# Kernel tuning notes

Measured on AMD Instinct MI355X. Metric: run time of the kernel, lower is better.

Reference implementation:

```python
import jax, jax.numpy as jnp
import numpy as np

B, C, H, W = 1, 512, 64, 64
HEADS, DH = 8, 64
DI = HEADS * DH          # 512 = heads * dim_head
SW = 8                   # sliding window size
CB = 16                  # compress block size
SB = 2                   # selection block size
NSEL = 2                 # num selected blocks
N = H * W                # 4096 tokens
NCB = N // CB            # 256 compress blocks
NFB = N // SB            # 2048 fine (selection) blocks
NEG = jnp.finfo(jnp.float32).min


def setup_inputs() -> dict:
    key = jax.random.key(0)
    ks = jax.random.split(key, 24)
    rn = lambda k, shape, s=0.03: jax.random.normal(k, shape, jnp.float32) * s
    return dict(
        x=jax.random.normal(ks[0], (B, C, H, W), jnp.float32),
        w_in=rn(ks[1], (C, C)), b_in=jnp.zeros((C,), jnp.float32),
        g_norm=jnp.ones((C,), jnp.float32),
        wq=rn(ks[2], (DI, C)), wk=rn(ks[3], (DI, C)), wv=rn(ks[4], (DI, C)),
        k_pos=rn(ks[5], (HEADS, CB, DH), 0.02), v_pos=rn(ks[6], (HEADS, CB, DH), 0.02),
        mem_k=rn(ks[7], (HEADS, 1, DH), 0.02), mem_v=rn(ks[8], (HEADS, 1, DH), 0.02),
        kc_w1=rn(ks[9], (CB * DH, CB * DH)), kc_b1=jnp.zeros((CB * DH,), jnp.float32),
        kc_w2=rn(ks[10], (DH, CB * DH)), kc_b2=jnp.zeros((DH,), jnp.float32),
        vc_w1=rn(ks[11], (CB * DH, CB * DH)), vc_b1=jnp.zeros((CB * DH,), jnp.float32),
        vc_w2=rn(ks[12], (DH, CB * DH)), vc_b2=jnp.zeros((DH,), jnp.float32),
        w_strat=rn(ks[13], (3 * HEADS, C)), b_strat=jnp.zeros((3 * HEADS,), jnp.float32),
        w_comb=rn(ks[14], (C, DI)),
        w_out=rn(ks[15], (C, C)), b_out=jnp.zeros((C,), jnp.float32),
    )


def _rope(x):
    # rotary-embedding-torch default: theta=10000, interleaved pairs
    d = x.shape[-1]
    inv = 1.0 / (10000.0 ** (jnp.arange(0, d, 2, dtype=jnp.float32) / d))
    ang = jnp.arange(x.shape[-2], dtype=jnp.float32)[:, None] * inv  # (n, d/2)
    cos = jnp.repeat(jnp.cos(ang), 2, axis=-1)
    sin = jnp.repeat(jnp.sin(ang), 2, axis=-1)
    xp = x.reshape(x.shape[:-1] + (d // 2, 2))
    xr = jnp.stack((-xp[..., 1], xp[..., 0]), axis=-1).reshape(x.shape)
    return x * cos + xr * sin


def reference(x, w_in, b_in, g_norm, wq, wk, wv, k_pos, v_pos, mem_k, mem_v,
              kc_w1, kc_b1, kc_w2, kc_b2, vc_w1, vc_b1, vc_w2, vc_b2,
              w_strat, b_strat, w_comb, w_out, b_out):
    scale = DH ** -0.5
    # proj_in (1x1 conv) then flatten to sequence (b, n, c); residual uses this
    xs = jnp.einsum('bchw,oc->bohw', x, w_in) + b_in[None, :, None, None]
    seq = xs.reshape(B, C, N).transpose(0, 2, 1)
    # RMSNorm
    h = seq * jax.lax.rsqrt(jnp.mean(seq * seq, -1, keepdims=True) + 1e-6) * g_norm
    # qkv -> (b, heads, n, d)
    q = (h @ wq.T).reshape(B, N, HEADS, DH).transpose(0, 2, 1, 3)
    k = (h @ wk.T).reshape(B, N, HEADS, DH).transpose(0, 2, 1, 3)
    v = (h @ wv.T).reshape(B, N, HEADS, DH).transpose(0, 2, 1, 3)

    # ---- 1. compressed attention (block compression MLP + mem kv) ----
    kin = (k + jnp.tile(k_pos, (1, NCB, 1))[None]).reshape(B, HEADS, NCB, CB * DH)
    vin = (v + jnp.tile(v_pos, (1, NCB, 1))[None]).reshape(B, HEADS, NCB, CB * DH)
    ck = jax.nn.relu(kin @ kc_w1.T + kc_b1) @ kc_w2.T + kc_b2   # (b,h,NCB,d)
    cv = jax.nn.relu(vin @ vc_w1.T + vc_b1) @ vc_w2.T + vc_b2
    ck = jnp.concatenate([jnp.broadcast_to(mem_k[None], (B, HEADS, 1, DH)), ck], axis=2)
    cv = jnp.concatenate([jnp.broadcast_to(mem_v[None], (B, HEADS, 1, DH)), cv], axis=2)
    ck_seq = jnp.concatenate([jnp.array([-1]), (jnp.arange(NCB) + 1) * CB - 1])
    cmask = ck_seq[None, :] < jnp.arange(N)[:, None]             # (N, NCB+1), True=attend
    csim = jnp.einsum('bhid,bhjd->bhij', q, ck) * scale
    csim = jnp.where(cmask[None, None], csim, NEG)
    compressed_out = jnp.einsum('bhij,bhjd->bhid', jax.nn.softmax(csim, axis=-1), cv)

    # rotary positions for fine + sliding branches
    rq, rk = _rope(q), _rope(k)

    # ---- 2. fine selection attention ----
    # importance at fine-block granularity; since SB divides CB, each fine block
    # maps to exactly one compress block (equivalent to repeat->mask->mean in torch)
    imp = csim[..., 1:]                                          # drop mem kv logits
    fb_of = jnp.arange(NFB) // (CB // SB)
    imp_fine = imp[..., fb_of]                                   # (b,h,N,NFB)
    blk_causal = jnp.arange(NFB)[None, :] < (jnp.arange(N) // SB)[:, None]
    imp_fine = jnp.where(blk_causal[None, None], imp_fine, -jnp.inf)
    logits = jnp.concatenate([jnp.full((B, HEADS, N, 1), -1e3, jnp.float32), imp_fine], axis=-1)
    probs = jax.nn.softmax(logits, axis=-1)[..., 1:]             # (b,h,N,NFB)
    sel_val, sel_idx = jax.lax.top_k(probs, NSEL)                # (b,h,N,NSEL)
    diag_idx = jnp.broadcast_to((jnp.arange(N) // SB)[None, None, :, None], (B, HEADS, N, 1))
    sel_idx = jnp.concatenate([sel_idx, diag_idx], axis=-1)      # append own (diagonal) block
    fmask_sel = jnp.repeat((sel_val > 1e-10)[..., None], SB, axis=-1)   # (b,h,N,NSEL,SB)
    diag_mask = jnp.arange(SB)[None, :] <= (jnp.arange(N) % SB)[:, None]  # within-block causal
    diag_mask = jnp.broadcast_to(diag_mask[None, None, :, None, :], (B, HEADS, N, 1, SB))
    fmask = jnp.concatenate([fmask_sel, diag_mask], axis=-2).reshape(B, HEADS, N, (NSEL + 1) * SB)
    fk_blk = rk.reshape(B, HEADS, NFB, SB, DH)
    fv_blk = v.reshape(B, HEADS, NFB, SB, DH)
    idx = sel_idx.reshape(B, HEADS, N * (NSEL + 1))[..., None, None]
    fk = jnp.take_along_axis(fk_blk, idx, axis=2).reshape(B, HEADS, N, (NSEL + 1) * SB, DH)
    fv = jnp.take_along_axis(fv_blk, idx, axis=2).reshape(B, HEADS, N, (NSEL + 1) * SB, DH)
    fsim = jnp.einsum('bhid,bhijd->bhij', rq, fk) * scale
    fsim = jnp.where(fmask, fsim, NEG)
    fine_out = jnp.einsum('bhij,bhijd->bhid', jax.nn.softmax(fsim, axis=-1), fv)

    # ---- 3. sliding window attention (causal, exact window: 0 <= i-j <= SW) ----
    kp = jnp.pad(rk, ((0, 0), (0, 0), (SW, 0), (0, 0)))
    vp = jnp.pad(v, ((0, 0), (0, 0), (SW, 0), (0, 0)))
    widx = jnp.arange(N)[:, None] + jnp.arange(SW + 1)[None, :]  # indices into padded seq
    kw = kp[:, :, widx]                                          # (b,h,N,SW+1,d)
    vw = vp[:, :, widx]
    wvalid = (jnp.arange(N)[:, None] - SW + jnp.arange(SW + 1)[None, :]) >= 0
    ssim = jnp.einsum('bhid,bhijd->bhij', rq, kw) * scale
    ssim = jnp.where(wvalid[None, None], ssim, NEG)
    slide_out = jnp.einsum('bhij,bhijd->bhid', jax.nn.softmax(ssim, axis=-1), vw)

    # ---- combine the three strategies with learned sigmoid gates ----
    gates = jax.nn.sigmoid(h @ w_strat.T + b_strat).reshape(B, N, HEADS, 3).transpose(0, 2, 1, 3)
    out = gates[..., 0:1] * compressed_out + gates[..., 1:2] * fine_out + gates[..., 2:3] * slide_out
    out = out.transpose(0, 2, 1, 3).reshape(B, N, DI) @ w_comb.T  # merge heads + combine
    out2d = out.transpose(0, 2, 1).reshape(B, C, H, W)
    return jnp.einsum('bchw,oc->bohw', out2d, w_out) + b_out[None, :, None, None] + xs
```

## Files before the change

kernel.cpp:

```cpp
#include <hip/hip_runtime.h>
#include <hip/hip_bf16.h>
#include <math.h>

typedef __attribute__((ext_vector_type(8))) short s8v;
typedef __attribute__((ext_vector_type(8))) _Float16 h8v;
typedef __attribute__((ext_vector_type(4))) float f4v;
typedef __hip_bfloat16 bf16;

#define NEGF (-3.40282346638528859812e+38f)
#define QSMEM 20480
#define BSMEM 20480

enum { EPI_F32 = 0, EPI_BIAS, EPI_BRELU_BF16, EPI_BF16, EPI_FINAL };

__device__ __forceinline__ float wred_sum(float v) {
#pragma unroll
  for (int m = 1; m < 64; m <<= 1) v += __shfl_xor(v, m, 64);
  return v;
}

template <int EPI>
__device__ __forceinline__ void bgemm_body(char* smem, int bx, int by, int bz,
    const bf16* __restrict__ A, const bf16* __restrict__ B, void* __restrict__ C,
    int K, int ldC, long sA, long sB, long sC,
    const float* __restrict__ bias, const void* __restrict__ aux) {
  short (*Ahs)[2560] = (short(*)[2560])smem;
  short (*Bhs)[2560] = (short(*)[2560])(smem + 2 * 2560 * 2);
  const short* ah = (const short*)A + (long)bz * sA;
  const short* bh = (const short*)B + (long)bz * sB;
  int tid = threadIdx.x;
  int wv_ = tid >> 6, lane = tid & 63;
  int lrow = tid >> 2, lcol = (tid & 3) << 3;
  int lidx = lrow * 40 + lcol;
  long abase = (long)(bx * 64 + lrow) * K + lcol;
  long bbase = (long)(by * 64 + lrow) * K + lcol;
  int frow = lane & 15, fk = (lane >> 4) << 3;
  int aoff = (wv_ * 16 + frow) * 40 + fk;
  f4v acc[4] = {};
  {
    s8v avh = *(const s8v*)&ah[abase];
    s8v bvh = *(const s8v*)&bh[bbase];
    *(s8v*)&Ahs[0][lidx] = avh;
    *(s8v*)&Bhs[0][lidx] = bvh;
  }
  __syncthreads();
  int nit = K >> 5, buf = 0;
  s8v rAa, rAb, rBa, rBb;
  if (nit > 1) {
    rAa = *(const s8v*)&ah[abase + 32];
    rAb = *(const s8v*)&bh[bbase + 32];
  }
#define B_DSMFMA                                                       \
  {                                                                    \
    s8v afh = *(const s8v*)&Ahs[buf][aoff];                            \
    _Pragma("unroll") for (int nt = 0; nt < 4; nt++) {                 \
      s8v bfh = *(const s8v*)&Bhs[buf][(nt * 16 + frow) * 40 + fk];    \
      acc[nt] = __builtin_amdgcn_mfma_f32_16x16x32_bf16(afh, bfh, acc[nt], 0, 0, 0); \
    }                                                                  \
  }
  for (int it = 0; it < nit; it += 2) {
    if (it + 2 < nit) {
      long ko = (long)(it + 2) << 5;
      rBa = *(const s8v*)&ah[abase + ko];
      rBb = *(const s8v*)&bh[bbase + ko];
    }
    B_DSMFMA
    if (it + 1 < nit) {
      *(s8v*)&Ahs[buf ^ 1][lidx] = rAa;
      *(s8v*)&Bhs[buf ^ 1][lidx] = rAb;
      __syncthreads();
      buf ^= 1;
      if (it + 3 < nit) {
        long ko = (long)(it + 3) << 5;
        rAa = *(const s8v*)&ah[abase + ko];
        rAb = *(const s8v*)&bh[bbase + ko];
      }
      B_DSMFMA
      if (it + 2 < nit) {
        *(s8v*)&Ahs[buf ^ 1][lidx] = rBa;
        *(s8v*)&Bhs[buf ^ 1][lidx] = rBb;
        __syncthreads();
        buf ^= 1;
      }
    }
  }
#undef B_DSMFMA
  int rb = bx * 64 + wv_ * 16 + ((lane >> 4) << 2);
#pragma unroll
  for (int nt = 0; nt < 4; nt++) {
    int gn = by * 64 + nt * 16 + (lane & 15);
#pragma unroll
    for (int rg = 0; rg < 4; rg++) {
      int gm = rb + rg;
      float v = acc[nt][rg];
      long ci = (long)bz * sC + (long)gm * ldC + gn;
      if (EPI == EPI_F32) ((float*)C)[ci] = v;
      else if (EPI == EPI_BIAS) ((float*)C)[ci] = v + bias[gn];
      else if (EPI == EPI_BRELU_BF16) ((bf16*)C)[ci] = __float2bfloat16(fmaxf(v + bias[gn], 0.f));
      else if (EPI == EPI_BF16) ((bf16*)C)[ci] = __float2bfloat16(v);
      else if (EPI == EPI_FINAL)
        ((float*)C)[ci] = v + bias[gm] + ((const float*)aux)[(long)gn * 512 + gm];
    }
  }
}


#define HX_DECL                                                     \
  short* L = (short*)smem;                                          \
  const int MS = 64 * 40;                                           \
  int tid = threadIdx.x;                                            \
  int wv = tid >> 6, lane = tid & 63;                               \
  int lrow = tid >> 2, lcol = (tid & 3) << 3;                       \
  int frow = lane & 15, fk = (lane >> 4) << 3;                      \
  int aoff = (wv * 16 + frow) * 40 + fk;                            \
  int soff = lrow * 40 + lcol;                                      \
  f4v acc0[4] = {}, accx[4] = {}, acc2[4] = {};

#define HX_STAGE0                                                   \
  {                                                                 \
    *(h8v*)&L[0 * MS + soff] = *(const h8v*)&Ah[abase];             \
    *(h8v*)&L[1 * MS + soff] = *(const h8v*)&Al[abase];             \
    *(h8v*)&L[2 * MS + soff] = *(const h8v*)&Bh[bbase];             \
    *(h8v*)&L[3 * MS + soff] = *(const h8v*)&Bl[bbase];             \
  }                                                                 \
  __syncthreads();

#define HX_DSMFMA                                                   \
  {                                                                 \
    h8v ah = *(const h8v*)&L[aoff];                                 \
    h8v al = *(const h8v*)&L[MS + aoff];                            \
    _Pragma("unroll") for (int nt = 0; nt < 4; nt++) {              \
      int bo = 2 * MS + (nt * 16 + frow) * 40 + fk;                 \
      h8v bh = *(const h8v*)&L[bo];                                 \
      h8v bl = *(const h8v*)&L[bo + MS];                            \
      acc0[nt] = __builtin_amdgcn_mfma_f32_16x16x32_f16(ah, bh, acc0[nt], 0, 0, 0); \
      accx[nt] = __builtin_amdgcn_mfma_f32_16x16x32_f16(ah, bl, accx[nt], 0, 0, 0); \
      accx[nt] = __builtin_amdgcn_mfma_f32_16x16x32_f16(al, bh, accx[nt], 0, 0, 0); \
      acc2[nt] = __builtin_amdgcn_mfma_f32_16x16x32_f16(al, bl, acc2[nt], 0, 0, 0); \
    }                                                               \
  }

#define HX_LOOP(NIT)                                                \
  h8v rAa, rAb, rAc, rAd, rBa, rBb, rBc, rBd;                       \
  if ((NIT) > 1) {                                                  \
    rAa = *(const h8v*)&Ah[abase + 32];                             \
    rAb = *(const h8v*)&Al[abase + 32];                             \
    rAc = *(const h8v*)&Bh[bbase + 32];                             \
    rAd = *(const h8v*)&Bl[bbase + 32];                             \
  }                                                                 \
  for (int it = 0; it < (NIT); it += 2) {                           \
    if (it + 2 < (NIT)) {                                           \
      long ko = (long)(it + 2) << 5;                                \
      rBa = *(const h8v*)&Ah[abase + ko];                           \
      rBb = *(const h8v*)&Al[abase + ko];                           \
      rBc = *(const h8v*)&Bh[bbase + ko];                           \
      rBd = *(const h8v*)&Bl[bbase + ko];                           \
    }                                                               \
    HX_DSMFMA                                                       \
    if (it + 1 < (NIT)) {                                           \
      __syncthreads();                                              \
      *(h8v*)&L[soff] = rAa;                                        \
      *(h8v*)&L[MS + soff] = rAb;                                   \
      *(h8v*)&L[2 * MS + soff] = rAc;                               \
      *(h8v*)&L[3 * MS + soff] = rAd;                               \
      __syncthreads();                                              \
      if (it + 3 < (NIT)) {                                         \
        long ko = (long)(it + 3) << 5;                              \
        rAa = *(const h8v*)&Ah[abase + ko];                         \
        rAb = *(const h8v*)&Al[abase + ko];                         \
        rAc = *(const h8v*)&Bh[bbase + ko];                         \
        rAd = *(const h8v*)&Bl[bbase + ko];                         \
      }                                                             \
      HX_DSMFMA                                                     \
      if (it + 2 < (NIT)) {                                         \
        __syncthreads();                                            \
        *(h8v*)&L[soff] = rBa;                                      \
        *(h8v*)&L[MS + soff] = rBb;                                 \
        *(h8v*)&L[2 * MS + soff] = rBc;                             \
        *(h8v*)&L[3 * MS + soff] = rBd;                             \
        __syncthreads();                                            \
      }                                                             \
    }                                                               \
  }

#define HX_COMBINE(nt, rg) \
  (acc0[nt][rg] + (accx[nt][rg] + acc2[nt][rg] * (1.f / 4096.f)) * (1.f / 4096.f))

__device__ __forceinline__ void qk_f16_body(char* smem, int bx, int by,
    const _Float16* __restrict__ Ah, const _Float16* __restrict__ Al,
    const _Float16* __restrict__ Bh, const _Float16* __restrict__ Bl,
    _Float16* __restrict__ qhh, _Float16* __restrict__ qhl,
    _Float16* __restrict__ kinh, _Float16* __restrict__ kinl,
    float* __restrict__ rq, float* __restrict__ rk, const float* __restrict__ kpos,
    const float2* __restrict__ ropet) {
  HX_DECL
  long abase = (long)(bx * 64 + lrow) * 512 + lcol;
  long bbase = (long)(by * 64 + lrow) * 512 + lcol;
  HX_STAGE0
  HX_LOOP(16)
  bool isq = by < 8;
  int h = by & 7;
  int rb = wv * 16 + ((lane >> 4) << 2);
#pragma unroll
  for (int nt = 0; nt < 4; nt++) {
    int dloc = nt * 16 + frow;
    int d2 = dloc >> 1;
#pragma unroll
    for (int rg = 0; rg < 4; rg++) {
      int n = bx * 64 + rb + rg;
      float vf = HX_COMBINE(nt, rg);
      float2 cs = ropet[(long)n * 32 + d2];
      float sv = cs.x, cv = cs.y;
      float vp = __shfl_xor(vf, 1, 64);
      float rr = (dloc & 1) ? (vf * cv + vp * sv) : (vf * cv - vp * sv);
      long oi = ((long)h * 4096 + n) * 64 + dloc;
      if (isq) {
        _Float16 hi = (_Float16)vf;
        qhh[oi] = hi;
        qhl[oi] = (_Float16)((vf - (float)hi) * 4096.f);
        rq[oi] = rr;
      } else {
        rk[oi] = rr;
        float kv = vf + kpos[(h * 16 + (n & 15)) * 64 + dloc];
        _Float16 khi = (_Float16)kv;
        long ki = (((long)h * 256 + (n >> 4)) * 16 + (n & 15)) * 64 + dloc;
        kinh[ki] = khi;
        kinl[ki] = (_Float16)((kv - (float)khi) * 4096.f);
      }
    }
  }
}

__device__ __forceinline__ void hx_conv_body(char* smem, int bx, int by,
    const _Float16* __restrict__ Ah, const _Float16* __restrict__ Al,
    const _Float16* __restrict__ Bh, const _Float16* __restrict__ Bl,
    float* __restrict__ C, const float* __restrict__ bias) {
  HX_DECL
  long abase = (long)(bx * 64 + lrow) * 512 + lcol;
  long bbase = (long)(by * 64 + lrow) * 512 + lcol;
  HX_STAGE0
  HX_LOOP(16)
  int rb = bx * 64 + wv * 16 + ((lane >> 4) << 2);
#pragma unroll
  for (int nt = 0; nt < 4; nt++) {
    int gn = by * 64 + nt * 16 + frow;
#pragma unroll
    for (int rg = 0; rg < 4; rg++) {
      int gm = rb + rg;
      C[(long)gm * 512 + gn] = HX_COMBINE(nt, rg) + bias[gn];
    }
  }
}

__device__ __forceinline__ void hx_mlp1_body(char* smem, int bx, int by,
    const _Float16* __restrict__ Ah, const _Float16* __restrict__ Al,
    const _Float16* __restrict__ Bh, const _Float16* __restrict__ Bl,
    _Float16* __restrict__ Ch, _Float16* __restrict__ Cl, const float* __restrict__ bias) {
  HX_DECL
  long abase = (long)(bx * 64 + lrow) * 1024 + lcol;
  long bbase = (long)(by * 64 + lrow) * 1024 + lcol;
  HX_STAGE0
  HX_LOOP(32)
  int rb = bx * 64 + wv * 16 + ((lane >> 4) << 2);
#pragma unroll
  for (int nt = 0; nt < 4; nt++) {
    int gn = by * 64 + nt * 16 + frow;
#pragma unroll
    for (int rg = 0; rg < 4; rg++) {
      int gm = rb + rg;
      float v = fmaxf(HX_COMBINE(nt, rg) + bias[gn], 0.f);
      _Float16 hi = (_Float16)v;
      long ci = (long)gm * 1024 + gn;
      Ch[ci] = hi;
      Cl[ci] = (_Float16)((v - (float)hi) * 4096.f);
    }
  }
}

__device__ __forceinline__ void hx_ksplit_body(char* smem, int bx, int by,
    const _Float16* __restrict__ Ah, const _Float16* __restrict__ Al,
    const _Float16* __restrict__ Bh, const _Float16* __restrict__ Bl,
    float* __restrict__ P) {
  HX_DECL
  long kbeg = (long)by << 7;
  long abase = (long)(bx * 64 + lrow) * 1024 + kbeg + lcol;
  long bbase = (long)lrow * 1024 + kbeg + lcol;
  HX_STAGE0
  HX_LOOP(4)
  float* p = P + (long)by * 131072;
  int rb = bx * 64 + wv * 16 + ((lane >> 4) << 2);
#pragma unroll
  for (int nt = 0; nt < 4; nt++) {
    int gn = nt * 16 + frow;
#pragma unroll
    for (int rg = 0; rg < 4; rg++) {
      int gm = rb + rg;
      p[(long)gm * 64 + gn] = HX_COMBINE(nt, rg);
    }
  }
}

__device__ __forceinline__ void hx_csim_body(char* smem, int bx, int by, int bz,
    const _Float16* __restrict__ Ah, const _Float16* __restrict__ Al,
    const _Float16* __restrict__ Bh, const _Float16* __restrict__ Bl,
    float* __restrict__ C) {
  HX_DECL
  long abase = ((long)bz * 4096 + bx * 64 + lrow) * 64 + lcol;
  long bbase = ((long)bz * 320 + by * 64 + lrow) * 64 + lcol;
  HX_STAGE0
  HX_LOOP(2)
  int rb = bx * 64 + wv * 16 + ((lane >> 4) << 2);
#pragma unroll
  for (int nt = 0; nt < 4; nt++) {
    int gn = by * 64 + nt * 16 + frow;
#pragma unroll
    for (int rg = 0; rg < 4; rg++) {
      int gm = rb + rg;
      C[((long)bz * 4096 + gm) * 320 + gn] = HX_COMBINE(nt, rg) * 0.125f;
    }
  }
}

__device__ __forceinline__ void prep_elem(long i,
    const float* __restrict__ wq, const float* __restrict__ wk, const float* __restrict__ wv,
    const float* __restrict__ wst, const float* __restrict__ bst,
    const float* __restrict__ kc_w1, const float* __restrict__ kc_w2,
    const float* __restrict__ vc_w1, const float* __restrict__ vc_w2, const float* __restrict__ w_comb,
    const float* __restrict__ w_out, _Float16* __restrict__ wqkh, _Float16* __restrict__ wqkl,
    bf16* __restrict__ wvs, float* __restrict__ bias2,
    _Float16* __restrict__ kw1h, _Float16* __restrict__ kw1l,
    _Float16* __restrict__ kw2h, _Float16* __restrict__ kw2l, bf16* __restrict__ vw1b,
    bf16* __restrict__ vw2b, bf16* __restrict__ wcombb, bf16* __restrict__ woutb) {
  if (i < 524288) {
    int r = (int)(i >> 9), c = (int)(i & 511);
    float w = (r < 512) ? wq[i] : wk[(r - 512) * 512 + c];
    _Float16 hi = (_Float16)w;
    wqkh[i] = hi;
    wqkl[i] = (_Float16)((w - (float)hi) * 4096.f);
    return;
  }
  i -= 524288;
  if (i < 294912) {
    int r = (int)(i >> 9), c = (int)(i & 511);
    float v = 0.f;
    if (r < 512) v = wv[i];
    else if (r < 536) v = wst[(r - 512) * 512 + c];
    wvs[i] = __float2bfloat16(v);
    if (i < 576) bias2[i] = (i >= 512 && i < 536) ? bst[i - 512] : 0.f;
    return;
  }
  i -= 294912;
  if (i < 1048576) {
    float w = kc_w1[i];
    _Float16 hi = (_Float16)w;
    kw1h[i] = hi;
    kw1l[i] = (_Float16)((w - (float)hi) * 4096.f);
    return;
  }
  i -= 1048576;
  if (i < 65536) {
    float w = kc_w2[i];
    _Float16 hi = (_Float16)w;
    kw2h[i] = hi;
    kw2l[i] = (_Float16)((w - (float)hi) * 4096.f);
    return;
  }
  i -= 65536;
  if (i < 1048576) { vw1b[i] = __float2bfloat16(vc_w1[i]); return; }
  i -= 1048576;
  if (i < 65536) { vw2b[i] = __float2bfloat16(vc_w2[i]); return; }
  i -= 65536;
  if (i < 262144) { wcombb[i] = __float2bfloat16(w_comb[i]); return; }
  i -= 262144;
  if (i < 262144) woutb[i] = __float2bfloat16(w_out[i]);
}
#define PREP_TOTAL 3571712l

template <int EPI>
__global__ __launch_bounds__(256) void gemm_bt(
    const bf16* __restrict__ A, const bf16* __restrict__ B, void* __restrict__ C,
    int K, int ldC, long sA, long sB, long sC,
    const float* __restrict__ bias, const void* __restrict__ aux) {
  __shared__ char smem[BSMEM];
  bgemm_body<EPI>(smem, blockIdx.x, blockIdx.y, blockIdx.z, A, B, C, K, ldC, sA, sB, sC, bias, aux);
}

__global__ __launch_bounds__(256) void k_conv_prep(
    const _Float16* __restrict__ xth, const _Float16* __restrict__ xtl,
    const _Float16* __restrict__ winh, const _Float16* __restrict__ winl,
    float* __restrict__ xsf, const float* __restrict__ b_in,
    const float* __restrict__ wq, const float* __restrict__ wk, const float* __restrict__ wv,
    const float* __restrict__ wst, const float* __restrict__ bst,
    const float* __restrict__ kc_w1, const float* __restrict__ kc_w2,
    const float* __restrict__ vc_w1, const float* __restrict__ vc_w2, const float* __restrict__ w_comb,
    const float* __restrict__ w_out, _Float16* __restrict__ wqkh, _Float16* __restrict__ wqkl,
    bf16* __restrict__ wvs, float* __restrict__ bias2,
    _Float16* __restrict__ kw1h, _Float16* __restrict__ kw1l,
    _Float16* __restrict__ kw2h, _Float16* __restrict__ kw2l, bf16* __restrict__ vw1b,
    bf16* __restrict__ vw2b, bf16* __restrict__ wcombb, bf16* __restrict__ woutb) {
  __shared__ char smem[QSMEM];
  if (blockIdx.y < 8) {
    hx_conv_body(smem, blockIdx.x, blockIdx.y, xth, xtl, winh, winl, xsf, b_in);
  } else {
    long base = (((long)(blockIdx.y - 8) * 64 + blockIdx.x) * 256) + threadIdx.x;
    for (long i = base; i < PREP_TOTAL; i += 16l * 64 * 256)
      prep_elem(i, wq, wk, wv, wst, bst, kc_w1, kc_w2, vc_w1, vc_w2, w_comb, w_out,
                wqkh, wqkl, wvs, bias2, kw1h, kw1l, kw2h, kw2l, vw1b, vw2b, wcombb, woutb);
  }
}

__global__ __launch_bounds__(256) void k_fused_qk_t2(
    const _Float16* __restrict__ hhi, const _Float16* __restrict__ hlo,
    const _Float16* __restrict__ wqkh, const _Float16* __restrict__ wqkl,
    _Float16* __restrict__ qhh, _Float16* __restrict__ qhl,
    _Float16* __restrict__ kinh, _Float16* __restrict__ kinl,
    float* __restrict__ rq, float* __restrict__ rk, const float* __restrict__ kpos,
    const float2* __restrict__ ropet,
    const bf16* __restrict__ hbf, const bf16* __restrict__ wvs, float* __restrict__ T2,
    const float* __restrict__ bias2) {
  __shared__ char smem[QSMEM];
  if (blockIdx.y >= 16) {
    bgemm_body<EPI_BIAS>(smem, blockIdx.x, blockIdx.y - 16, 0, hbf, wvs, T2, 512, 576, 0, 0, 0, bias2,
                         nullptr);
    return;
  }
  qk_f16_body(smem, blockIdx.x, blockIdx.y, hhi, hlo, wqkh, wqkl, qhh, qhl, kinh, kinl, rq, rk, kpos,
              ropet);
}

__global__ void k_repackV(const float* __restrict__ T2, const float* __restrict__ vpos,
                          float* __restrict__ vvv, bf16* __restrict__ vin) {
  int e = blockIdx.x * 256 + threadIdx.x;
  int d = e & 63, n = (e >> 6) & 4095, h = e >> 18;
  float v0 = T2[(long)n * 576 + h * 64 + d];
  vvv[((long)h * 4096 + n) * 64 + d] = v0;
  vin[(((long)h * 256 + (n >> 4)) * 16 + (n & 15)) * 64 + d] =
      __float2bfloat16(v0 + vpos[(h * 16 + (n & 15)) * 64 + d]);
}

__global__ __launch_bounds__(256) void k_fused_mlp1(
    const _Float16* __restrict__ kinh, const _Float16* __restrict__ kinl,
    const _Float16* __restrict__ kw1h, const _Float16* __restrict__ kw1l,
    _Float16* __restrict__ hidh, _Float16* __restrict__ hidl, const float* __restrict__ kb1,
    const bf16* __restrict__ vin, const bf16* __restrict__ vw1,
    bf16* __restrict__ hidv, const float* __restrict__ vb1) {
  __shared__ char smem[QSMEM];
  if (blockIdx.y < 16)
    hx_mlp1_body(smem, blockIdx.x, blockIdx.y, kinh, kinl, kw1h, kw1l, hidh, hidl, kb1);
  else
    bgemm_body<EPI_BRELU_BF16>(smem, blockIdx.x, blockIdx.y - 16, 0, vin, vw1, hidv, 1024, 1024, 0, 0, 0,
                               vb1, nullptr);
}

__global__ __launch_bounds__(256) void k_fused_mlp2(
    const _Float16* __restrict__ hidh, const _Float16* __restrict__ hidl,
    const _Float16* __restrict__ kw2h, const _Float16* __restrict__ kw2l, float* __restrict__ kpart,
    const bf16* __restrict__ hidv, const bf16* __restrict__ vw2, float* __restrict__ cvc,
    const float* __restrict__ vb2) {
  __shared__ char smem[QSMEM];
  if (blockIdx.y < 8)
    hx_ksplit_body(smem, blockIdx.x, blockIdx.y, hidh, hidl, kw2h, kw2l, kpart);
  else
    bgemm_body<EPI_BIAS>(smem, blockIdx.x, 0, 0, hidv, vw2, cvc, 1024, 64, 0, 0, 0, vb2, nullptr);
}

__global__ __launch_bounds__(256) void k_csim(
    const _Float16* __restrict__ qhh, const _Float16* __restrict__ qhl,
    const _Float16* __restrict__ ckbh, const _Float16* __restrict__ ckbl, float* __restrict__ csim) {
  if (blockIdx.y * 64 > blockIdx.x * 4 + 3) return;
  __shared__ char smem[QSMEM];
  hx_csim_body(smem, blockIdx.x, blockIdx.y, blockIdx.z, qhh, qhl, ckbh, ckbl, csim);
}

__global__ void k_transpose16(const float* __restrict__ x, _Float16* __restrict__ xth,
                              _Float16* __restrict__ xtl,
                              const float* __restrict__ w_in, _Float16* __restrict__ winh,
                              _Float16* __restrict__ winl, float2* __restrict__ ropet) {
  if (blockIdx.y == 16) {
    int tid = threadIdx.y * 32 + threadIdx.x;
    long base = (long)blockIdx.x * 256 + tid;
    for (long i = base; i < 393216; i += 128l * 256) {
      if (i < 262144) {
        float w = w_in[i];
        _Float16 hi = (_Float16)w;
        winh[i] = hi;
        winl[i] = (_Float16)((w - (float)hi) * 4096.f);
      } else {
        int idx = (int)(i - 262144);
        int d2 = idx & 31, n = idx >> 5;
        float inv = exp2f((float)d2 * -0.4152410118609203f);
        float sv, cv;
        sincosf((float)n * inv, &sv, &cv);
        ropet[idx] = make_float2(sv, cv);
      }
    }
    return;
  }
  __shared__ float t[32][33];
  int n0 = blockIdx.x * 32, c0 = blockIdx.y * 32;
  int tx = threadIdx.x, ty = threadIdx.y;
#pragma unroll
  for (int r = ty; r < 32; r += 8) t[r][tx] = x[(long)(c0 + r) * 4096 + n0 + tx];
  __syncthreads();
#pragma unroll
  for (int r = ty; r < 32; r += 8) {
    float v = t[tx][r];
    _Float16 hi = (_Float16)v;
    long o = (long)(n0 + r) * 512 + c0 + tx;
    xth[o] = hi;
    xtl[o] = (_Float16)((v - (float)hi) * 4096.f);
  }
}

__global__ __launch_bounds__(256) void k_rmsnorm(const float* __restrict__ xs, const float* __restrict__ g,
                                                 _Float16* __restrict__ hhi, _Float16* __restrict__ hlo,
                                                 bf16* __restrict__ hbf) {
  int n = blockIdx.x, t = threadIdx.x;
  const float* row = xs + (long)n * 512;
  double a = (double)row[t], b = (double)row[t + 256];
  double ss = a * a + b * b;
#pragma unroll
  for (int m = 1; m < 64; m <<= 1) ss += __shfl_xor(ss, m, 64);
  __shared__ double red[4];
  if ((t & 63) == 0) red[t >> 6] = ss;
  __syncthreads();
  double tot = red[0] + red[1] + red[2] + red[3];
  double r = 1.0 / sqrt(tot / 512.0 + 1e-6);
  double h0 = a * r * (double)g[t], h1 = b * r * (double)g[t + 256];
  long o = (long)n * 512 + t;
  float f0 = (float)h0, f1 = (float)h1;
  _Float16 a0 = (_Float16)f0, a1 = (_Float16)f1;
  hhi[o] = a0;
  hhi[o + 256] = a1;
  hlo[o] = (_Float16)((f0 - (float)a0) * 4096.f);
  hlo[o + 256] = (_Float16)((f1 - (float)a1) * 4096.f);
  hbf[o] = __float2bfloat16(f0);
  hbf[o + 256] = __float2bfloat16(f1);
}

__global__ void k_repackB(const float* __restrict__ kpart, const float* __restrict__ cvc,
                          const float* __restrict__ mem_k, const float* __restrict__ mem_v,
                          const float* __restrict__ kb2, _Float16* __restrict__ ckbh,
                          _Float16* __restrict__ ckbl, bf16* __restrict__ cvtb) {
  int g = blockIdx.x * 256 + threadIdx.x;
  if (g < 8 * 320 * 64) {
    int d = g & 63, j = (g >> 6) % 320, h = g / (320 * 64);
    float vf = 0.f;
    if (j == 0) vf = mem_k[h * 64 + d];
    else if (j < 257) {
      long ri = ((long)h * 256 + (j - 1)) * 64 + d;
      double s = 0.0;
#pragma unroll
      for (int p = 0; p < 8; p++) s += (double)kpart[(long)p * 131072 + ri];
      vf = (float)(s + (double)kb2[d]);
    }
    _Float16 hi = (_Float16)vf;
    ckbh[g] = hi;
    ckbl[g] = (_Float16)((vf - (float)hi) * 4096.f);
  }
  if (g < 8 * 64 * 288) {
    int j = g % 288, d = (g / 288) & 63, h = g / (288 * 64);
    float v = 0.f;
    if (j == 0) v = mem_v[h * 64 + d];
    else if (j < 257) v = cvc[((long)h * 256 + (j - 1)) * 64 + d];
    cvtb[g] = __float2bfloat16(v);
  }
}

__global__ __launch_bounds__(256) void k_selsm(const float* __restrict__ csim, bf16* __restrict__ pb,
                                               int4* __restrict__ selb) {
  int r = blockIdx.x * 4 + (threadIdx.x >> 6);
  int lane = threadIdx.x & 63;
  int i = r & 4095;
  const float* row = csim + (long)r * 320;
  int nv = i / 16 + 1;
  float s[5], e[5];
  float mx = -INFINITY;
#pragma unroll
  for (int t = 0; t < 5; t++) {
    int j = lane + 64 * t;
    float v = (j < nv) ? row[j] : -INFINITY;
    s[t] = v;
    mx = fmaxf(mx, v);
  }
#pragma unroll
  for (int m = 1; m < 64; m <<= 1) mx = fmaxf(mx, __shfl_xor(mx, m, 64));
  float sum = 0.f;
#pragma unroll
  for (int t = 0; t < 5; t++) {
    int j = lane + 64 * t;
    e[t] = (j < nv) ? __expf(s[t] - mx) : 0.f;
    sum += e[t];
  }
  sum = wred_sum(sum);
  float rinv = 1.f / sum;
  bf16* prow = pb + (long)r * 288;
#pragma unroll
  for (int t = 0; t < 5; t++) {
    int j = lane + 64 * t;
    if (j < 288) prow[j] = __float2bfloat16((j < nv) ? e[t] * rinv : 0.f);
  }
  int nvb = i >> 1;
  int nmv = (nvb + 7) >> 3;
  float vm[4];
  float bestv = -INFINITY;
  int bestm = 0x7fffffff;
#pragma unroll
  for (int t = 0; t < 4; t++) {
    int m = lane + 64 * t;
    float v = -INFINITY;
    if (m < nmv) v = (m + 1 < nv) ? row[m + 1] : NEGF;
    vm[t] = v;
    if (v > bestv) { bestv = v; bestm = m; }
  }
#pragma unroll
  for (int mk = 1; mk < 64; mk <<= 1) {
    float ov = __shfl_xor(bestv, mk, 64);
    int om = __shfl_xor(bestm, mk, 64);
    if (ov > bestv || (ov == bestv && om < bestm)) { bestv = ov; bestm = om; }
  }
  int m0 = bestm;
  int cnt0 = min(8, nvb - 8 * m0);
  float rv = -INFINITY;
  int rm = 0x7fffffff;
#pragma unroll
  for (int t = 0; t < 4; t++) {
    int m = lane + 64 * t;
    if (m != m0 && vm[t] > rv) { rv = vm[t]; rm = m; }
  }
#pragma unroll
  for (int mk = 1; mk < 64; mk <<= 1) {
    float ov = __shfl_xor(rv, mk, 64);
    int om = __shfl_xor(rm, mk, 64);
    if (ov > rv || (ov == rv && om < rm)) { rv = ov; rm = om; }
  }
  float Ml = fmaxf(-1000.f, bestv);
  float z = 0.f;
#pragma unroll
  for (int t = 0; t < 4; t++) {
    int m = lane + 64 * t;
    if (m < nmv) z += (float)min(8, nvb - 8 * m) * expf(vm[t] - Ml);
  }
  z = wred_sum(z) + expf(-1000.f - Ml);
  int fb0 = 0, fb1 = 0, mk0 = 0, mk1 = 0;
  if (nmv > 0) {
    float sv0 = expf(bestv - Ml) / z;
    fb0 = 8 * m0;
    mk0 = sv0 > 1e-10f;
    if (cnt0 >= 2) { fb1 = fb0 + 1; mk1 = mk0; }
    else if (nmv > 1) {
      float sv1 = expf(rv - Ml) / z;
      fb1 = 8 * rm;
      mk1 = sv1 > 1e-10f;
    }
  }
  if (lane == 0) selb[r] = make_int4(fb0, fb1, mk0, mk1);
}

__global__ __launch_bounds__(256) void k_fineslide(const float* __restrict__ rq, const float* __restrict__ rk,
                                                   const float* __restrict__ vv, const float* __restrict__ co,
                                                   const int4* __restrict__ selb, const float* __restrict__ T2,
                                                   bf16* __restrict__ comb) {
  int r = blockIdx.x * 4 + (threadIdx.x >> 6);
  int d = threadIdx.x & 63;
  int h = r >> 12, i = r & 4095;
  long hb = (long)h * 4096 * 64;
  float qd = rq[hb + (long)i * 64 + d];
  int4 s4 = selb[r];
  int dg = i >> 1;
  int tok[6] = {2 * s4.x, 2 * s4.x + 1, 2 * s4.y, 2 * s4.y + 1, 2 * dg, 2 * dg + 1};
  int ok6[6] = {s4.z, s4.z, s4.w, s4.w, 1, (i & 1)};
  float sim[6], val[6];
#pragma unroll
  for (int j = 0; j < 6; j++) {
    float kd = rk[hb + (long)tok[j] * 64 + d];
    val[j] = vv[hb + (long)tok[j] * 64 + d];
    float p = wred_sum(qd * kd);
    sim[j] = ok6[j] ? p * 0.125f : NEGF;
  }
  float mx = sim[0];
#pragma unroll
  for (int j = 1; j < 6; j++) mx = fmaxf(mx, sim[j]);
  float den = 0.f, fo = 0.f;
#pragma unroll
  for (int j = 0; j < 6; j++) {
    float e_ = __expf(sim[j] - mx);
    den += e_;
    fo += e_ * val[j];
  }
  fo /= den;
  float ssim[9], sval[9];
#pragma unroll
  for (int t = 0; t < 9; t++) {
    int tk = i - 8 + t;
    int okt = tk >= 0;
    int tc = okt ? tk : 0;
    float kd = rk[hb + (long)tc * 64 + d];
    sval[t] = okt ? vv[hb + (long)tc * 64 + d] : 0.f;
    float p = wred_sum(qd * kd);
    ssim[t] = okt ? p * 0.125f : NEGF;
  }
  float mx2 = ssim[8];
#pragma unroll
  for (int t = 0; t < 8; t++) mx2 = fmaxf(mx2, ssim[t]);
  float den2 = 0.f, so = 0.f;
#pragma unroll
  for (int t = 0; t < 9; t++) {
    float e_ = __expf(ssim[t] - mx2);
    den2 += e_;
    so += e_ * sval[t];
  }
  so /= den2;
  const float* gb = T2 + (long)i * 576 + 512 + h * 3;
  float g0 = 1.f / (1.f + __expf(-gb[0]));
  float g1 = 1.f / (1.f + __expf(-gb[1]));
  float g2 = 1.f / (1.f + __expf(-gb[2]));
  float cd = co[hb + (long)i * 64 + d];
  comb[(long)i * 512 + h * 64 + d] = __float2bfloat16(g0 * cd + g1 * fo + g2 * so);
}

extern "C" void kernel_launch(void* const* d_in, const int* in_sizes, int n_in, void* d_out, int out_size,
                              void* d_ws, size_t ws_size, hipStream_t stream) {
  (void)in_sizes; (void)n_in; (void)out_size; (void)ws_size;
  const float* x = (const float*)d_in[0];
  const float* w_in = (const float*)d_in[1];
  const float* b_in = (const float*)d_in[2];
  const float* g_norm = (const float*)d_in[3];
  const float* wq = (const float*)d_in[4];
  const float* wk = (const float*)d_in[5];
  const float* wv = (const float*)d_in[6];
  const float* k_pos = (const float*)d_in[7];
  const float* v_pos = (const float*)d_in[8];
  const float* mem_k = (const float*)d_in[9];
  const float* mem_v = (const float*)d_in[10];
  const float* kc_w1 = (const float*)d_in[11];
  const float* kc_b1 = (const float*)d_in[12];
  const float* kc_w2 = (const float*)d_in[13];
  const float* kc_b2 = (const float*)d_in[14];
  const float* vc_w1 = (const float*)d_in[15];
  const float* vc_b1 = (const float*)d_in[16];
  const float* vc_w2 = (const float*)d_in[17];
  const float* vc_b2 = (const float*)d_in[18];
  const float* w_strat = (const float*)d_in[19];
  const float* b_strat = (const float*)d_in[20];
  const float* w_comb = (const float*)d_in[21];
  const float* w_out = (const float*)d_in[22];
  const float* b_out = (const float*)d_in[23];

  char* wsp = (char*)d_ws;
  size_t off = 0;
  auto alloc = [&](size_t b) -> void* {
    void* p = wsp + off;
    off += (b + 255) & ~(size_t)255;
    return p;
  };
  float* xsf = (float*)alloc(4096l * 512 * 4);
  _Float16* hhi = (_Float16*)alloc(4096l * 512 * 2);
  _Float16* hlo = (_Float16*)alloc(4096l * 512 * 2);
  bf16* hbf = (bf16*)alloc(4096l * 512 * 2);
  _Float16* winh = (_Float16*)alloc(512l * 512 * 2);
  _Float16* winl = (_Float16*)alloc(512l * 512 * 2);
  _Float16* wqkh = (_Float16*)alloc(1024l * 512 * 2);
  _Float16* wqkl = (_Float16*)alloc(1024l * 512 * 2);
  bf16* wvs = (bf16*)alloc(576l * 512 * 2);
  float* bias2 = (float*)alloc(576 * 4);
  float2* ropet = (float2*)alloc(4096l * 32 * 8);
  float* T2 = (float*)alloc(4096l * 576 * 4);
  float* csim = (float*)alloc(8l * 4096 * 320 * 4);
  _Float16* qhh = (_Float16*)alloc(8l * 4096 * 64 * 2);
  _Float16* qhl = (_Float16*)alloc(8l * 4096 * 64 * 2);
  float* rq = (float*)alloc(8l * 4096 * 64 * 4);
  float* rk = (float*)alloc(8l * 4096 * 64 * 4);
  float* vvb = (float*)alloc(8l * 4096 * 64 * 4);
  char* xthl = (char*)alloc(2l * 4096 * 512 * 2);
  _Float16* xth = (_Float16*)xthl;
  _Float16* xtl = xth + 4096l * 512;
  _Float16* hidh = xth;
  _Float16* hidl = xtl;
  char* kinpb = (char*)alloc(2048l * 1024 * 8 + 2048l * 1024 * 2);
  _Float16* kinh = (_Float16*)kinpb;
  _Float16* kinl = kinh + 2048l * 1024;
  bf16* vinb = (bf16*)(kinpb + 2l * 2048 * 1024 * 2);
  bf16* pb = (bf16*)kinpb;
  _Float16* kw1h = (_Float16*)alloc(1024l * 1024 * 2);
  _Float16* kw1l = (_Float16*)alloc(1024l * 1024 * 2);
  _Float16* kw2h = (_Float16*)alloc(64l * 1024 * 2);
  _Float16* kw2l = (_Float16*)alloc(64l * 1024 * 2);
  bf16* vw1b = (bf16*)alloc(1024l * 1024 * 2);
  bf16* vw2b = (bf16*)alloc(64l * 1024 * 2);
  bf16* hidv = (bf16*)alloc(2048l * 1024 * 2);
  float* cvc = (float*)alloc(2048l * 64 * 4);
  _Float16* ckbh = (_Float16*)alloc(8l * 320 * 64 * 2);
  _Float16* ckbl = (_Float16*)alloc(8l * 320 * 64 * 2);
  bf16* cvtb = (bf16*)alloc(8l * 64 * 288 * 2);
  int4* selb = (int4*)alloc(32768l * 16);
  float* co = (float*)alloc(8l * 4096 * 64 * 4);
  bf16* comb = (bf16*)alloc(4096l * 512 * 2);
  bf16* zb = (bf16*)alloc(4096l * 512 * 2);
  bf16* wcombb = (bf16*)alloc(512l * 512 * 2);
  bf16* woutb = (bf16*)alloc(512l * 512 * 2);
  float* kpart = (float*)alloc(8l * 2048 * 64 * 4);

  k_transpose16<<<dim3(128, 17), dim3(32, 8), 0, stream>>>(x, xth, xtl, w_in, winh, winl, ropet);
  k_conv_prep<<<dim3(64, 24), 256, 0, stream>>>(xth, xtl, winh, winl, xsf, b_in, wq, wk, wv, w_strat,
                                                b_strat, kc_w1, kc_w2, vc_w1, vc_w2, w_comb, w_out,
                                                wqkh, wqkl, wvs, bias2, kw1h, kw1l, kw2h, kw2l,
                                                vw1b, vw2b, wcombb, woutb);
  k_rmsnorm<<<4096, 256, 0, stream>>>(xsf, g_norm, hhi, hlo, hbf);
  k_fused_qk_t2<<<dim3(64, 25, 1), 256, 0, stream>>>(hhi, hlo, wqkh, wqkl, qhh, qhl, kinh, kinl, rq, rk,
                                                     k_pos, ropet, hbf, wvs, T2, bias2);
  k_repackV<<<8192, 256, 0, stream>>>(T2, v_pos, vvb, vinb);
  k_fused_mlp1<<<dim3(32, 32, 1), 256, 0, stream>>>(kinh, kinl, kw1h, kw1l, hidh, hidl, kc_b1, vinb, vw1b,
                                                    hidv, vc_b1);
  k_fused_mlp2<<<dim3(32, 9, 1), 256, 0, stream>>>(hidh, hidl, kw2h, kw2l, kpart, hidv, vw2b, cvc, vc_b2);
  k_repackB<<<640, 256, 0, stream>>>(kpart, cvc, mem_k, mem_v, kc_b2, ckbh, ckbl, cvtb);
  k_csim<<<dim3(64, 5, 8), 256, 0, stream>>>(qhh, qhl, ckbh, ckbl, csim);
  k_selsm<<<8192, 256, 0, stream>>>(csim, pb, selb);
  gemm_bt<EPI_F32><<<dim3(64, 1, 8), 256, 0, stream>>>(pb, cvtb, co, 288, 64, 4096l * 288, 64l * 288,
                                                       4096l * 64, nullptr, nullptr);
  k_fineslide<<<8192, 256, 0, stream>>>(rq, rk, vvb, co, selb, T2, comb);
  gemm_bt<EPI_BF16><<<dim3(64, 8, 1), 256, 0, stream>>>(comb, wcombb, zb, 512, 512, 0, 0, 0, nullptr, nullptr);
  gemm_bt<EPI_FINAL><<<dim3(8, 64, 1), 256, 0, stream>>>(woutb, zb, d_out, 512, 4096, 0, 0, 0, b_out, xsf);
}
```

Baseline: 325.6 us.

## Fuse compressed-similarity GEMM into selection softmax kernel and deepen MLP2 k-split

Removes the separate csim GEMM kernel and its large fp32 csim buffer. The selection/softmax kernel now computes each 16-row query tile's similarities directly with split-f16 MFMAs into shared memory, then runs the softmax and top-block selection from LDS. This avoids writing and re-reading a roughly 42 MB intermediate, at the cost of fewer MFMA tiles per wave and per-row serial work inside each block. Separately, the k-split for the second key-compression MLP is doubled from 8 to 16 partitions for more parallelism, which means more partial sums for repackB to reduce.

```diff
diff --git a/kernel.cpp b/kernel.cpp
--- a/kernel.cpp
+++ b/kernel.cpp
@@ -178,7 +178,7 @@
         *(h8v*)&L[MS + soff] = rBb;                                 \
         *(h8v*)&L[2 * MS + soff] = rBc;                             \
         *(h8v*)&L[3 * MS + soff] = rBd;                             \
-        __syncthreads();                                            \
+      __syncthreads();                                              \
       }                                                             \
     }                                                               \
   }
@@ -282,11 +282,11 @@
     const _Float16* __restrict__ Bh, const _Float16* __restrict__ Bl,
     float* __restrict__ P) {
   HX_DECL
-  long kbeg = (long)by << 7;
+  long kbeg = (long)by << 6;
   long abase = (long)(bx * 64 + lrow) * 1024 + kbeg + lcol;
   long bbase = (long)lrow * 1024 + kbeg + lcol;
   HX_STAGE0
-  HX_LOOP(4)
+  HX_LOOP(2)
   float* p = P + (long)by * 131072;
   int rb = bx * 64 + wv * 16 + ((lane >> 4) << 2);
 #pragma unroll
@@ -296,27 +296,6 @@
     for (int rg = 0; rg < 4; rg++) {
       int gm = rb + rg;
       p[(long)gm * 64 + gn] = HX_COMBINE(nt, rg);
-    }
-  }
-}
-
-__device__ __forceinline__ void hx_csim_body(char* smem, int bx, int by, int bz,
-    const _Float16* __restrict__ Ah, const _Float16* __restrict__ Al,
-    const _Float16* __restrict__ Bh, const _Float16* __restrict__ Bl,
-    float* __restrict__ C) {
-  HX_DECL
-  long abase = ((long)bz * 4096 + bx * 64 + lrow) * 64 + lcol;
-  long bbase = ((long)bz * 320 + by * 64 + lrow) * 64 + lcol;
-  HX_STAGE0
-  HX_LOOP(2)
-  int rb = bx * 64 + wv * 16 + ((lane >> 4) << 2);
-#pragma unroll
-  for (int nt = 0; nt < 4; nt++) {
-    int gn = by * 64 + nt * 16 + frow;
-#pragma unroll
-    for (int rg = 0; rg < 4; rg++) {
-      int gm = rb + rg;
-      C[((long)bz * 4096 + gm) * 320 + gn] = HX_COMBINE(nt, rg) * 0.125f;
     }
   }
 }
@@ -458,18 +437,10 @@
     const bf16* __restrict__ hidv, const bf16* __restrict__ vw2, float* __restrict__ cvc,
     const float* __restrict__ vb2) {
   __shared__ char smem[QSMEM];
-  if (blockIdx.y < 8)
+  if (blockIdx.y < 16)
     hx_ksplit_body(smem, blockIdx.x, blockIdx.y, hidh, hidl, kw2h, kw2l, kpart);
   else
     bgemm_body<EPI_BIAS>(smem, blockIdx.x, 0, 0, hidv, vw2, cvc, 1024, 64, 0, 0, 0, vb2, nullptr);
-}
-
-__global__ __launch_bounds__(256) void k_csim(
-    const _Float16* __restrict__ qhh, const _Float16* __restrict__ qhl,
-    const _Float16* __restrict__ ckbh, const _Float16* __restrict__ ckbl, float* __restrict__ csim) {
-  if (blockIdx.y * 64 > blockIdx.x * 4 + 3) return;
-  __shared__ char smem[QSMEM];
-  hx_csim_body(smem, blockIdx.x, blockIdx.y, blockIdx.z, qhh, qhl, ckbh, ckbl, csim);
 }
 
 __global__ void k_transpose16(const float* __restrict__ x, _Float16* __restrict__ xth,
@@ -551,7 +522,7 @@
       long ri = ((long)h * 256 + (j - 1)) * 64 + d;
       double s = 0.0;
 #pragma unroll
-      for (int p = 0; p < 8; p++) s += (double)kpart[(long)p * 131072 + ri];
+      for (int p = 0; p < 16; p++) s += (double)kpart[(long)p * 131072 + ri];
       vf = (float)(s + (double)kb2[d]);
     }
     _Float16 hi = (_Float16)vf;
@@ -567,94 +538,127 @@
   }
 }
 
-__global__ __launch_bounds__(256) void k_selsm(const float* __restrict__ csim, bf16* __restrict__ pb,
-                                               int4* __restrict__ selb) {
-  int r = blockIdx.x * 4 + (threadIdx.x >> 6);
-  int lane = threadIdx.x & 63;
-  int i = r & 4095;
-  const float* row = csim + (long)r * 320;
-  int nv = i / 16 + 1;
-  float s[5], e[5];
-  float mx = -INFINITY;
-#pragma unroll
-  for (int t = 0; t < 5; t++) {
-    int j = lane + 64 * t;
-    float v = (j < nv) ? row[j] : -INFINITY;
-    s[t] = v;
-    mx = fmaxf(mx, v);
-  }
-#pragma unroll
-  for (int m = 1; m < 64; m <<= 1) mx = fmaxf(mx, __shfl_xor(mx, m, 64));
-  float sum = 0.f;
-#pragma unroll
-  for (int t = 0; t < 5; t++) {
-    int j = lane + 64 * t;
-    e[t] = (j < nv) ? __expf(s[t] - mx) : 0.f;
-    sum += e[t];
-  }
-  sum = wred_sum(sum);
-  float rinv = 1.f / sum;
-  bf16* prow = pb + (long)r * 288;
-#pragma unroll
-  for (int t = 0; t < 5; t++) {
-    int j = lane + 64 * t;
-    if (j < 288) prow[j] = __float2bfloat16((j < nv) ? e[t] * rinv : 0.f);
-  }
-  int nvb = i >> 1;
-  int nmv = (nvb + 7) >> 3;
-  float vm[4];
-  float bestv = -INFINITY;
-  int bestm = 0x7fffffff;
-#pragma unroll
-  for (int t = 0; t < 4; t++) {
-    int m = lane + 64 * t;
-    float v = -INFINITY;
-    if (m < nmv) v = (m + 1 < nv) ? row[m + 1] : NEGF;
-    vm[t] = v;
-    if (v > bestv) { bestv = v; bestm = m; }
-  }
-#pragma unroll
-  for (int mk = 1; mk < 64; mk <<= 1) {
-    float ov = __shfl_xor(bestv, mk, 64);
-    int om = __shfl_xor(bestm, mk, 64);
-    if (ov > bestv || (ov == bestv && om < bestm)) { bestv = ov; bestm = om; }
-  }
-  int m0 = bestm;
-  int cnt0 = min(8, nvb - 8 * m0);
-  float rv = -INFINITY;
-  int rm = 0x7fffffff;
-#pragma unroll
-  for (int t = 0; t < 4; t++) {
-    int m = lane + 64 * t;
-    if (m != m0 && vm[t] > rv) { rv = vm[t]; rm = m; }
-  }
-#pragma unroll
-  for (int mk = 1; mk < 64; mk <<= 1) {
-    float ov = __shfl_xor(rv, mk, 64);
-    int om = __shfl_xor(rm, mk, 64);
-    if (ov > rv || (ov == rv && om < rm)) { rv = ov; rm = om; }
-  }
-  float Ml = fmaxf(-1000.f, bestv);
-  float z = 0.f;
-#pragma unroll
-  for (int t = 0; t < 4; t++) {
-    int m = lane + 64 * t;
-    if (m < nmv) z += (float)min(8, nvb - 8 * m) * expf(vm[t] - Ml);
-  }
-  z = wred_sum(z) + expf(-1000.f - Ml);
-  int fb0 = 0, fb1 = 0, mk0 = 0, mk1 = 0;
-  if (nmv > 0) {
-    float sv0 = expf(bestv - Ml) / z;
-    fb0 = 8 * m0;
-    mk0 = sv0 > 1e-10f;
-    if (cnt0 >= 2) { fb1 = fb0 + 1; mk1 = mk0; }
-    else if (nmv > 1) {
-      float sv1 = expf(rv - Ml) / z;
-      fb1 = 8 * rm;
-      mk1 = sv1 > 1e-10f;
-    }
-  }
-  if (lane == 0) selb[r] = make_int4(fb0, fb1, mk0, mk1);
+__global__ __launch_bounds__(256) void k_selsm(
+    const _Float16* __restrict__ qhh, const _Float16* __restrict__ qhl,
+    const _Float16* __restrict__ ckbh, const _Float16* __restrict__ ckbl,
+    bf16* __restrict__ pb, int4* __restrict__ selb) {
+  __shared__ float S[16][337];
+  int bx = blockIdx.x, h = blockIdx.y;
+  int tid = threadIdx.x, wv = tid >> 6, lane = tid & 63;
+  int nv = bx + 1;
+  int ntile = (nv + 15) >> 4;
+  int frow = lane & 15, fkh = (lane >> 4) << 3;
+  long qbase = ((long)h * 4096 + bx * 16 + frow) * 64 + fkh;
+  h8v qh0 = *(const h8v*)&qhh[qbase];
+  h8v ql0 = *(const h8v*)&qhl[qbase];
+  h8v qh1 = *(const h8v*)&qhh[qbase + 32];
+  h8v ql1 = *(const h8v*)&qhl[qbase + 32];
+  for (int jt = wv; jt < ntile; jt += 4) {
+    long bbase = ((long)h * 320 + jt * 16 + frow) * 64 + fkh;
+    h8v bh0 = *(const h8v*)&ckbh[bbase];
+    h8v bl0 = *(const h8v*)&ckbl[bbase];
+    h8v bh1 = *(const h8v*)&ckbh[bbase + 32];
+    h8v bl1 = *(const h8v*)&ckbl[bbase + 32];
+    f4v a0 = {}, ax = {};
+    a0 = __builtin_amdgcn_mfma_f32_16x16x32_f16(qh0, bh0, a0, 0, 0, 0);
+    ax = __builtin_amdgcn_mfma_f32_16x16x32_f16(qh0, bl0, ax, 0, 0, 0);
+    ax = __builtin_amdgcn_mfma_f32_16x16x32_f16(ql0, bh0, ax, 0, 0, 0);
+    a0 = __builtin_amdgcn_mfma_f32_16x16x32_f16(qh1, bh1, a0, 0, 0, 0);
+    ax = __builtin_amdgcn_mfma_f32_16x16x32_f16(qh1, bl1, ax, 0, 0, 0);
+    ax = __builtin_amdgcn_mfma_f32_16x16x32_f16(ql1, bh1, ax, 0, 0, 0);
+#pragma unroll
+    for (int rg = 0; rg < 4; rg++)
+      S[(lane >> 4) * 4 + rg][jt * 16 + (lane & 15)] =
+          (a0[rg] + ax[rg] * (1.f / 4096.f)) * 0.125f;
+  }
+  __syncthreads();
+  for (int rr = 0; rr < 4; rr++) {
+    int lr = wv * 4 + rr;
+    int i = bx * 16 + lr;
+    long r = (long)h * 4096 + i;
+    const float* row = S[lr];
+    float s[5], e[5];
+    float mx = -INFINITY;
+#pragma unroll
+    for (int t = 0; t < 5; t++) {
+      int j = lane + 64 * t;
+      float v = (j < nv) ? row[j] : -INFINITY;
+      s[t] = v;
+      mx = fmaxf(mx, v);
+    }
+#pragma unroll
+    for (int m = 1; m < 64; m <<= 1) mx = fmaxf(mx, __shfl_xor(mx, m, 64));
+    float sum = 0.f;
+#pragma unroll
+    for (int t = 0; t < 5; t++) {
+      int j = lane + 64 * t;
+      e[t] = (j < nv) ? __expf(s[t] - mx) : 0.f;
+      sum += e[t];
+    }
+    sum = wred_sum(sum);
+    float rinv = 1.f / sum;
+    bf16* prow = pb + (long)r * 288;
+#pragma unroll
+    for (int t = 0; t < 5; t++) {
+      int j = lane + 64 * t;
+      if (j < 288) prow[j] = __float2bfloat16((j < nv) ? e[t] * rinv : 0.f);
+    }
+    int nvb = i >> 1;
+    int nmv = (nvb + 7) >> 3;
+    float vm[4];
+    float bestv = -INFINITY;
+    int bestm = 0x7fffffff;
+#pragma unroll
+    for (int t = 0; t < 4; t++) {
+      int m = lane + 64 * t;
+      float v = -INFINITY;
+      if (m < nmv) v = (m + 1 < nv) ? row[m + 1] : NEGF;
+      vm[t] = v;
+      if (v > bestv) { bestv = v; bestm = m; }
+    }
+#pragma unroll
+    for (int mk = 1; mk < 64; mk <<= 1) {
+      float ov = __shfl_xor(bestv, mk, 64);
+      int om = __shfl_xor(bestm, mk, 64);
+      if (ov > bestv || (ov == bestv && om < bestm)) { bestv = ov; bestm = om; }
+    }
+    int m0 = bestm;
+    int cnt0 = min(8, nvb - 8 * m0);
+    float rv = -INFINITY;
+    int rm = 0x7fffffff;
+#pragma unroll
+    for (int t = 0; t < 4; t++) {
+      int m = lane + 64 * t;
+      if (m != m0 && vm[t] > rv) { rv = vm[t]; rm = m; }
+    }
+#pragma unroll
+    for (int mk = 1; mk < 64; mk <<= 1) {
+      float ov = __shfl_xor(rv, mk, 64);
+      int om = __shfl_xor(rm, mk, 64);
+      if (ov > rv || (ov == rv && om < rm)) { rv = ov; rm = om; }
+    }
+    float Ml = fmaxf(-1000.f, bestv);
+    float z = 0.f;
+#pragma unroll
+    for (int t = 0; t < 4; t++) {
+      int m = lane + 64 * t;
+      if (m < nmv) z += (float)min(8, nvb - 8 * m) * expf(vm[t] - Ml);
+    }
+    z = wred_sum(z) + expf(-1000.f - Ml);
+    int fb0 = 0, fb1 = 0, mk0 = 0, mk1 = 0;
+    if (nmv > 0) {
+      float sv0 = expf(bestv - Ml) / z;
+      fb0 = 8 * m0;
+      mk0 = sv0 > 1e-10f;
+      if (cnt0 >= 2) { fb1 = fb0 + 1; mk1 = mk0; }
+      else if (nmv > 1) {
+        float sv1 = expf(rv - Ml) / z;
+        fb1 = 8 * rm;
+        mk1 = sv1 > 1e-10f;
+      }
+    }
+    if (lane == 0) selb[r] = make_int4(fb0, fb1, mk0, mk1);
+  }
 }
 
 __global__ __launch_bounds__(256) void k_fineslide(const float* __restrict__ rq, const float* __restrict__ rk,
@@ -766,7 +770,6 @@
   float* bias2 = (float*)alloc(576 * 4);
   float2* ropet = (float2*)alloc(4096l * 32 * 8);
   float* T2 = (float*)alloc(4096l * 576 * 4);
-  float* csim = (float*)alloc(8l * 4096 * 320 * 4);
   _Float16* qhh = (_Float16*)alloc(8l * 4096 * 64 * 2);
   _Float16* qhl = (_Float16*)alloc(8l * 4096 * 64 * 2);
   float* rq = (float*)alloc(8l * 4096 * 64 * 4);
@@ -799,7 +802,7 @@
   bf16* zb = (bf16*)alloc(4096l * 512 * 2);
   bf16* wcombb = (bf16*)alloc(512l * 512 * 2);
   bf16* woutb = (bf16*)alloc(512l * 512 * 2);
-  float* kpart = (float*)alloc(8l * 2048 * 64 * 4);
+  float* kpart = (float*)alloc(16l * 2048 * 64 * 4);
 
   k_transpose16<<<dim3(128, 17), dim3(32, 8), 0, stream>>>(x, xth, xtl, w_in, winh, winl, ropet);
   k_conv_prep<<<dim3(64, 24), 256, 0, stream>>>(xth, xtl, winh, winl, xsf, b_in, wq, wk, wv, w_strat,
@@ -812,10 +815,9 @@
   k_repackV<<<8192, 256, 0, stream>>>(T2, v_pos, vvb, vinb);
   k_fused_mlp1<<<dim3(32, 32, 1), 256, 0, stream>>>(kinh, kinl, kw1h, kw1l, hidh, hidl, kc_b1, vinb, vw1b,
                                                     hidv, vc_b1);
-  k_fused_mlp2<<<dim3(32, 9, 1), 256, 0, stream>>>(hidh, hidl, kw2h, kw2l, kpart, hidv, vw2b, cvc, vc_b2);
+  k_fused_mlp2<<<dim3(32, 17, 1), 256, 0, stream>>>(hidh, hidl, kw2h, kw2l, kpart, hidv, vw2b, cvc, vc_b2);
   k_repackB<<<640, 256, 0, stream>>>(kpart, cvc, mem_k, mem_v, kc_b2, ckbh, ckbl, cvtb);
-  k_csim<<<dim3(64, 5, 8), 256, 0, stream>>>(qhh, qhl, ckbh, ckbl, csim);
-  k_selsm<<<8192, 256, 0, stream>>>(csim, pb, selb);
+  k_selsm<<<dim3(256, 8), 256, 0, stream>>>(qhh, qhl, ckbh, ckbl, pb, selb);
   gemm_bt<EPI_F32><<<dim3(64, 1, 8), 256, 0, stream>>>(pb, cvtb, co, 288, 64, 4096l * 288, 64l * 288,
                                                        4096l * 64, nullptr, nullptr);
   k_fineslide<<<8192, 256, 0, stream>>>(rq, rk, vvb, co, selb, T2, comb);
```

After: 328.3 us. About the same (+0.8%).
